# Performance work log

Measured on AMD Instinct MI355X. Metric: run time of the kernel, lower is better.

## Reference

```python
import jax, jax.numpy as jnp
import numpy as np

B, S, H, D = 8, 4096, 16, 64  # head_dim D = hidden_dim // n_heads
HID = H * D
EPS = 1e-5

def _layernorm(x, w, b):
    mu = jnp.mean(x, axis=-1, keepdims=True)
    var = jnp.var(x, axis=-1, keepdims=True)
    return (x - mu) * jax.lax.rsqrt(var + EPS) * w + b

def setup_inputs() -> dict:
    key = jax.random.key(0)
    ks = jax.random.split(key, 14)
    s = 1.0 / np.sqrt(D)
    return {
        "queries": jax.random.normal(ks[0], (B, S, HID), jnp.float32),
        "keys": jax.random.normal(ks[1], (B, S, HID), jnp.float32),
        "values": jax.random.normal(ks[2], (B, S, HID), jnp.float32),
        "memorys": jax.random.normal(ks[3], (B, H, S, D), jnp.float32),
        "Wq": jax.random.uniform(ks[4], (D, D), jnp.float32, -s, s),
        "Wk": jax.random.uniform(ks[5], (D, D), jnp.float32, -s, s),
        "Wv": jax.random.uniform(ks[6], (D, D), jnp.float32, -s, s),
        "forget_gate": jax.random.normal(ks[7], (D,), jnp.float32),
        "ln1_w": jnp.ones((D,), jnp.float32),
        "ln1_b": jnp.zeros((D,), jnp.float32),
        "W1": jax.random.uniform(ks[8], (2 * D, D), jnp.float32, -s, s),
        "ln2_w": jnp.ones((2 * D,), jnp.float32),
        "ln2_b": jnp.zeros((2 * D,), jnp.float32),
        "W2": jax.random.uniform(ks[9], (D, 2 * D), jnp.float32, -1.0 / np.sqrt(2 * D), 1.0 / np.sqrt(2 * D)),
        "b2": jax.random.uniform(ks[10], (D,), jnp.float32, -1.0 / np.sqrt(2 * D), 1.0 / np.sqrt(2 * D)),
    }

def reference(queries, keys, values, memorys, Wq, Wk, Wv, forget_gate,
              ln1_w, ln1_b, W1, ln2_w, ln2_b, W2, b2):
    # [B,S,HID] -> [B,H,S,D]
    def split_heads(x):
        return jnp.transpose(x.reshape(B, S, H, D), (0, 2, 1, 3))
    q_ = jnp.einsum('bhsd,ed->bhse', split_heads(queries), Wq)
    k_ = jnp.einsum('bhsd,ed->bhse', split_heads(keys), Wk)
    v_ = jnp.einsum('bhsd,ed->bhse', split_heads(values), Wv)
    # elementwise forget-gate memory cell
    cell = k_ * v_ + forget_gate * memorys
    cur_mem = (1.0 - forget_gate) * cell + forget_gate * memorys
    cv = q_ * cur_mem  # [B,H,S,D]
    # token mixer: LN -> Linear(D->2D, no bias) -> LN -> Linear(2D->D, bias)
    h1 = jnp.einsum('bhsd,ed->bhse', _layernorm(cv, ln1_w, ln1_b), W1)
    mixed = jnp.einsum('bhse,de->bhsd', _layernorm(h1, ln2_w, ln2_b), W2) + b2
    out = jnp.transpose(mixed, (0, 2, 1, 3)).reshape(B, S, HID)
    return out, cur_mem
```

## Files before the change

kernel.cpp:

```cpp
#include <hip/hip_runtime.h>

typedef __attribute__((ext_vector_type(4))) float f32x4;
typedef __attribute__((ext_vector_type(8))) __bf16 bf16x8;

#define MFMA(a, b, c) __builtin_amdgcn_mfma_f32_16x16x32_bf16(a, b, c, 0, 0, 0)

__device__ __forceinline__ void wave_fence() {
  asm volatile("" ::: "memory");
  __builtin_amdgcn_wave_barrier();
  asm volatile("" ::: "memory");
}

__device__ __forceinline__ bf16x8 pack8(f32x4 a, f32x4 b) {
  bf16x8 r;
  r[0] = (__bf16)a[0]; r[1] = (__bf16)a[1]; r[2] = (__bf16)a[2]; r[3] = (__bf16)a[3];
  r[4] = (__bf16)b[0]; r[5] = (__bf16)b[1]; r[6] = (__bf16)b[2]; r[7] = (__bf16)b[3];
  return r;
}

constexpr int SD  = 262144;
constexpr int HSD = 4194304;

__global__ __launch_bounds__(256, 2) void mixer_kernel(
    const float* __restrict__ Qg, const float* __restrict__ Kg,
    const float* __restrict__ Vg, const float* __restrict__ Mg,
    const float* __restrict__ Wq, const float* __restrict__ Wk,
    const float* __restrict__ Wv, const float* __restrict__ FG,
    const float* __restrict__ L1W, const float* __restrict__ L1B,
    const float* __restrict__ W1, const float* __restrict__ L2W,
    const float* __restrict__ L2B, const float* __restrict__ W2,
    const float* __restrict__ B2g, float* __restrict__ Out,
    float* __restrict__ Cm) {
  __shared__ __attribute__((aligned(16))) __bf16 lds[24576];
  const int tid = threadIdx.x;
  const int wave = tid >> 6, lane = tid & 63;
  const int c = lane & 15, g = lane >> 4;

  for (int i = tid; i < 4096; i += 256) {
    const int j = i & 7, L = (i >> 3) & 63, t = i >> 9;
    const int k = ((t >> 2) << 5) + ((L >> 4) << 3) + j;
    const int n = ((t & 3) << 4) + (L & 15);
    lds[i]         = (__bf16)Wq[n * 64 + k];
    lds[4096 + i]  = (__bf16)Wk[n * 64 + k];
    lds[8192 + i]  = (__bf16)Wv[n * 64 + k];
  }
  for (int i = tid; i < 8192; i += 256) {
    const int j = i & 7, L = (i >> 3) & 63, t = i >> 9;
    const int k = ((t >> 3) << 5) + ((L >> 4) << 3) + j;
    const int n = ((t & 7) << 4) + (L & 15);
    lds[12288 + i] = (__bf16)W1[n * 64 + k];
  }
  __syncthreads();

  float fgv[4], l1wv[4], l1bv[4], b2v[4], l2wv[8], l2bv[8];
#pragma unroll
  for (int t = 0; t < 4; ++t) {
    fgv[t]  = FG[t * 16 + c];
    l1wv[t] = L1W[t * 16 + c];
    l1bv[t] = L1B[t * 16 + c];
    b2v[t]  = B2g[t * 16 + c];
  }
#pragma unroll
  for (int t = 0; t < 8; ++t) { l2wv[t] = L2W[t * 16 + c]; l2bv[t] = L2B[t * 16 + c]; }

  bf16x8 fb2[16];
#pragma unroll
  for (int kt = 0; kt < 4; ++kt)
#pragma unroll
    for (int nt = 0; nt < 4; ++nt) {
      const float* p = W2 + (nt * 16 + c) * 128 + kt * 32 + g * 8;
      f32x4 a = *(const f32x4*)p;
      f32x4 b = *(const f32x4*)(p + 4);
      fb2[kt * 4 + nt] = pack8(a, b);
    }

  const f32x4 zf = {0.f, 0.f, 0.f, 0.f};
  const int p0 = blockIdx.x * 32;

  for (int it = 0; it < 8; ++it) {
    const int pair = p0 + it * 4 + wave;
    const int bb = pair >> 12, s = pair & 4095;

    int lz = 0;
    asm volatile("" : "+s"(lz));
    const __bf16* wl = lds + lz;
    __bf16* stg = lds + 20480 + wave * 1024 + lz;

    const float* qp = Qg + pair * 1024;
    const float* kp = Kg + pair * 1024;
    const float* vp = Vg + pair * 1024;
    const int aoff = c * 64 + g * 8;

    const f32x4 q0 = *(const f32x4*)(qp + aoff);
    const f32x4 q1 = *(const f32x4*)(qp + aoff + 4);
    const f32x4 q2 = *(const f32x4*)(qp + aoff + 32);
    const f32x4 q3 = *(const f32x4*)(qp + aoff + 36);
    const f32x4 k0 = *(const f32x4*)(kp + aoff);
    const f32x4 k1 = *(const f32x4*)(kp + aoff + 4);
    const f32x4 k2 = *(const f32x4*)(kp + aoff + 32);
    const f32x4 k3 = *(const f32x4*)(kp + aoff + 36);
    const f32x4 v0 = *(const f32x4*)(vp + aoff);
    const f32x4 v1 = *(const f32x4*)(vp + aoff + 4);
    const f32x4 v2 = *(const f32x4*)(vp + aoff + 32);
    const f32x4 v3 = *(const f32x4*)(vp + aoff + 36);

    const int mb = bb * HSD + s * 64 + c;
    float mv[4][4];
#pragma unroll
    for (int nt = 0; nt < 4; ++nt)
#pragma unroll
      for (int r = 0; r < 4; ++r)
        mv[nt][r] = Mg[mb + (g * 4 + r) * SD + nt * 16];

    const bf16x8 aq0 = pack8(q0, q1), aq1 = pack8(q2, q3);
    const bf16x8 ak0 = pack8(k0, k1), ak1 = pack8(k2, k3);
    const bf16x8 av0 = pack8(v0, v1), av1 = pack8(v2, v3);

    f32x4 accq[4], acck[4], accv[4];
#pragma unroll
    for (int nt = 0; nt < 4; ++nt) { accq[nt] = zf; acck[nt] = zf; accv[nt] = zf; }

#pragma unroll
    for (int nt = 0; nt < 4; ++nt) {
      accq[nt] = MFMA(aq0, *(const bf16x8*)(wl + nt * 512 + lane * 8), accq[nt]);
      accq[nt] = MFMA(aq1, *(const bf16x8*)(wl + (4 + nt) * 512 + lane * 8), accq[nt]);
      acck[nt] = MFMA(ak0, *(const bf16x8*)(wl + 4096 + nt * 512 + lane * 8), acck[nt]);
      acck[nt] = MFMA(ak1, *(const bf16x8*)(wl + 4096 + (4 + nt) * 512 + lane * 8), acck[nt]);
      accv[nt] = MFMA(av0, *(const bf16x8*)(wl + 8192 + nt * 512 + lane * 8), accv[nt]);
      accv[nt] = MFMA(av1, *(const bf16x8*)(wl + 8192 + (4 + nt) * 512 + lane * 8), accv[nt]);
    }

    float cv[4][4];
#pragma unroll
    for (int nt = 0; nt < 4; ++nt) {
      const float f = fgv[nt];
#pragma unroll
      for (int r = 0; r < 4; ++r) {
        const float mm = mv[nt][r];
        const float cell = acck[nt][r] * accv[nt][r] + f * mm;
        const float cm = (1.f - f) * cell + f * mm;
        Cm[mb + (g * 4 + r) * SD + nt * 16] = cm;
        cv[nt][r] = accq[nt][r] * cm;
      }
    }

    float yv[4][4];
#pragma unroll
    for (int r = 0; r < 4; ++r) {
      float s1 = cv[0][r] + cv[1][r] + cv[2][r] + cv[3][r];
      float s2 = cv[0][r] * cv[0][r] + cv[1][r] * cv[1][r] + cv[2][r] * cv[2][r] + cv[3][r] * cv[3][r];
#pragma unroll
      for (int msk = 1; msk <= 8; msk <<= 1) {
        s1 += __shfl_xor(s1, msk);
        s2 += __shfl_xor(s2, msk);
      }
      const float mu = s1 * 0.015625f;
      const float var = s2 * 0.015625f - mu * mu;
      const float rstd = rsqrtf(var + 1e-5f);
#pragma unroll
      for (int nt = 0; nt < 4; ++nt)
        yv[nt][r] = (cv[nt][r] - mu) * rstd * l1wv[nt] + l1bv[nt];
    }

    wave_fence();
#pragma unroll
    for (int nt = 0; nt < 4; ++nt)
#pragma unroll
      for (int r = 0; r < 4; ++r) {
        const int m = g * 4 + r, k = nt * 16 + c;
        stg[(m << 6) + ((((k >> 3) ^ (m & 7)) << 3)) + (k & 7)] = (__bf16)yv[nt][r];
      }
    wave_fence();
    bf16x8 a2[2];
#pragma unroll
    for (int kt = 0; kt < 2; ++kt)
      a2[kt] = *(const bf16x8*)(stg + (c << 6) + ((((kt * 4 + g) ^ (c & 7)) << 3)));

    f32x4 acch[8];
#pragma unroll
    for (int j = 0; j < 8; ++j) acch[j] = zf;
#pragma unroll
    for (int kt = 0; kt < 2; ++kt)
#pragma unroll
      for (int nt = 0; nt < 8; ++nt)
        acch[nt] = MFMA(a2[kt], *(const bf16x8*)(wl + 12288 + (kt * 8 + nt) * 512 + lane * 8), acch[nt]);

    float zz[8][4];
#pragma unroll
    for (int r = 0; r < 4; ++r) {
      float s1 = 0.f, s2 = 0.f;
#pragma unroll
      for (int j = 0; j < 8; ++j) { const float x = acch[j][r]; s1 += x; s2 += x * x; }
#pragma unroll
      for (int msk = 1; msk <= 8; msk <<= 1) {
        s1 += __shfl_xor(s1, msk);
        s2 += __shfl_xor(s2, msk);
      }
      const float mu = s1 * 0.0078125f;
      const float var = s2 * 0.0078125f - mu * mu;
      const float rstd = rsqrtf(var + 1e-5f);
#pragma unroll
      for (int j = 0; j < 8; ++j)
        zz[j][r] = (acch[j][r] - mu) * rstd * l2wv[j] + l2bv[j];
    }

    f32x4 acco[4];
#pragma unroll
    for (int nt = 0; nt < 4; ++nt) acco[nt] = zf;
#pragma unroll
    for (int half = 0; half < 2; ++half) {
      wave_fence();
#pragma unroll
      for (int jj = 0; jj < 4; ++jj)
#pragma unroll
        for (int r = 0; r < 4; ++r) {
          const int m = g * 4 + r, k = jj * 16 + c;
          stg[(m << 6) + ((((k >> 3) ^ (m & 7)) << 3)) + (k & 7)] = (__bf16)zz[half * 4 + jj][r];
        }
      wave_fence();
#pragma unroll
      for (int kk = 0; kk < 2; ++kk) {
        const bf16x8 a3 = *(const bf16x8*)(stg + (c << 6) + ((((kk * 4 + g) ^ (c & 7)) << 3)));
#pragma unroll
        for (int nt = 0; nt < 4; ++nt)
          acco[nt] = MFMA(a3, fb2[(half * 2 + kk) * 4 + nt], acco[nt]);
      }
    }

    const int ob = pair * 1024;
#pragma unroll
    for (int nt = 0; nt < 4; ++nt)
#pragma unroll
      for (int r = 0; r < 4; ++r)
        Out[ob + (g * 4 + r) * 64 + nt * 16 + c] = acco[nt][r] + b2v[nt];
  }
}

extern "C" void kernel_launch(void* const* d_in, const int* in_sizes, int n_in,
                              void* d_out, int out_size, void* d_ws, size_t ws_size,
                              hipStream_t stream) {
  const float* Qg  = (const float*)d_in[0];
  const float* Kg  = (const float*)d_in[1];
  const float* Vg  = (const float*)d_in[2];
  const float* Mg  = (const float*)d_in[3];
  const float* Wq  = (const float*)d_in[4];
  const float* Wk  = (const float*)d_in[5];
  const float* Wv  = (const float*)d_in[6];
  const float* FG  = (const float*)d_in[7];
  const float* L1W = (const float*)d_in[8];
  const float* L1B = (const float*)d_in[9];
  const float* W1  = (const float*)d_in[10];
  const float* L2W = (const float*)d_in[11];
  const float* L2B = (const float*)d_in[12];
  const float* W2  = (const float*)d_in[13];
  const float* B2g = (const float*)d_in[14];
  float* Out = (float*)d_out;
  float* Cm  = Out + 33554432;

  mixer_kernel<<<dim3(1024), dim3(256), 0, stream>>>(
      Qg, Kg, Vg, Mg, Wq, Wk, Wv, FG, L1W, L1B, W1, L2W, L2B, W2, B2g, Out, Cm);
}
```

Baseline: 654.8 us.

## Prefetch next pair's Q/K/V/memory inputs and move W2 fragments to LDS

```diff
diff --git a/kernel.cpp b/kernel.cpp
--- a/kernel.cpp
+++ b/kernel.cpp
@@ -31,10 +31,34 @@
     const float* __restrict__ L2B, const float* __restrict__ W2,
     const float* __restrict__ B2g, float* __restrict__ Out,
     float* __restrict__ Cm) {
-  __shared__ __attribute__((aligned(16))) __bf16 lds[24576];
+  __shared__ __attribute__((aligned(16))) __bf16 lds[32768];
   const int tid = threadIdx.x;
   const int wave = tid >> 6, lane = tid & 63;
   const int c = lane & 15, g = lane >> 4;
+  const int aoff = c * 64 + g * 8;
+  const int p0 = blockIdx.x * 32;
+
+  int pair = p0 + wave;
+  f32x4 q0, q1, q2, q3, k0, k1, k2, k3, v0, v1, v2, v3;
+  float mv[4][4];
+  int mb;
+  {
+    const float* qp = Qg + pair * 1024;
+    const float* kp = Kg + pair * 1024;
+    const float* vp = Vg + pair * 1024;
+    q0 = *(const f32x4*)(qp + aoff);      q1 = *(const f32x4*)(qp + aoff + 4);
+    q2 = *(const f32x4*)(qp + aoff + 32); q3 = *(const f32x4*)(qp + aoff + 36);
+    k0 = *(const f32x4*)(kp + aoff);      k1 = *(const f32x4*)(kp + aoff + 4);
+    k2 = *(const f32x4*)(kp + aoff + 32); k3 = *(const f32x4*)(kp + aoff + 36);
+    v0 = *(const f32x4*)(vp + aoff);      v1 = *(const f32x4*)(vp + aoff + 4);
+    v2 = *(const f32x4*)(vp + aoff + 32); v3 = *(const f32x4*)(vp + aoff + 36);
+    mb = (pair >> 12) * HSD + (pair & 4095) * 64 + c;
+#pragma unroll
+    for (int nt = 0; nt < 4; ++nt)
+#pragma unroll
+      for (int r = 0; r < 4; ++r)
+        mv[nt][r] = Mg[mb + (g * 4 + r) * SD + nt * 16];
+  }
 
   for (int i = tid; i < 4096; i += 256) {
     const int j = i & 7, L = (i >> 3) & 63, t = i >> 9;
@@ -46,9 +70,12 @@
   }
   for (int i = tid; i < 8192; i += 256) {
     const int j = i & 7, L = (i >> 3) & 63, t = i >> 9;
-    const int k = ((t >> 3) << 5) + ((L >> 4) << 3) + j;
-    const int n = ((t & 7) << 4) + (L & 15);
-    lds[12288 + i] = (__bf16)W1[n * 64 + k];
+    const int k1 = ((t >> 3) << 5) + ((L >> 4) << 3) + j;
+    const int n1 = ((t & 7) << 4) + (L & 15);
+    lds[12288 + i] = (__bf16)W1[n1 * 64 + k1];
+    const int k2 = ((t >> 2) << 5) + ((L >> 4) << 3) + j;
+    const int n2 = ((t & 3) << 4) + (L & 15);
+    lds[20480 + i] = (__bf16)W2[n2 * 128 + k2];
   }
   __syncthreads();
 
@@ -63,58 +90,30 @@
 #pragma unroll
   for (int t = 0; t < 8; ++t) { l2wv[t] = L2W[t * 16 + c]; l2bv[t] = L2B[t * 16 + c]; }
 
-  bf16x8 fb2[16];
-#pragma unroll
-  for (int kt = 0; kt < 4; ++kt)
-#pragma unroll
-    for (int nt = 0; nt < 4; ++nt) {
-      const float* p = W2 + (nt * 16 + c) * 128 + kt * 32 + g * 8;
-      f32x4 a = *(const f32x4*)p;
-      f32x4 b = *(const f32x4*)(p + 4);
-      fb2[kt * 4 + nt] = pack8(a, b);
-    }
-
   const f32x4 zf = {0.f, 0.f, 0.f, 0.f};
-  const int p0 = blockIdx.x * 32;
 
   for (int it = 0; it < 8; ++it) {
-    const int pair = p0 + it * 4 + wave;
-    const int bb = pair >> 12, s = pair & 4095;
-
     int lz = 0;
     asm volatile("" : "+s"(lz));
     const __bf16* wl = lds + lz;
-    __bf16* stg = lds + 20480 + wave * 1024 + lz;
-
-    const float* qp = Qg + pair * 1024;
-    const float* kp = Kg + pair * 1024;
-    const float* vp = Vg + pair * 1024;
-    const int aoff = c * 64 + g * 8;
-
-    const f32x4 q0 = *(const f32x4*)(qp + aoff);
-    const f32x4 q1 = *(const f32x4*)(qp + aoff + 4);
-    const f32x4 q2 = *(const f32x4*)(qp + aoff + 32);
-    const f32x4 q3 = *(const f32x4*)(qp + aoff + 36);
-    const f32x4 k0 = *(const f32x4*)(kp + aoff);
-    const f32x4 k1 = *(const f32x4*)(kp + aoff + 4);
-    const f32x4 k2 = *(const f32x4*)(kp + aoff + 32);
-    const f32x4 k3 = *(const f32x4*)(kp + aoff + 36);
-    const f32x4 v0 = *(const f32x4*)(vp + aoff);
-    const f32x4 v1 = *(const f32x4*)(vp + aoff + 4);
-    const f32x4 v2 = *(const f32x4*)(vp + aoff + 32);
-    const f32x4 v3 = *(const f32x4*)(vp + aoff + 36);
-
-    const int mb = bb * HSD + s * 64 + c;
-    float mv[4][4];
-#pragma unroll
-    for (int nt = 0; nt < 4; ++nt)
-#pragma unroll
-      for (int r = 0; r < 4; ++r)
-        mv[nt][r] = Mg[mb + (g * 4 + r) * SD + nt * 16];
+    __bf16* stg = lds + 28672 + wave * 1024 + lz;
 
     const bf16x8 aq0 = pack8(q0, q1), aq1 = pack8(q2, q3);
     const bf16x8 ak0 = pack8(k0, k1), ak1 = pack8(k2, k3);
     const bf16x8 av0 = pack8(v0, v1), av1 = pack8(v2, v3);
+
+    if (it < 7) {
+      const int np = pair + 4;
+      const float* qn = Qg + np * 1024;
+      const float* kn = Kg + np * 1024;
+      const float* vn = Vg + np * 1024;
+      q0 = *(const f32x4*)(qn + aoff);      q1 = *(const f32x4*)(qn + aoff + 4);
+      q2 = *(const f32x4*)(qn + aoff + 32); q3 = *(const f32x4*)(qn + aoff + 36);
+      k0 = *(const f32x4*)(kn + aoff);      k1 = *(const f32x4*)(kn + aoff + 4);
+      k2 = *(const f32x4*)(kn + aoff + 32); k3 = *(const f32x4*)(kn + aoff + 36);
+      v0 = *(const f32x4*)(vn + aoff);      v1 = *(const f32x4*)(vn + aoff + 4);
+      v2 = *(const f32x4*)(vn + aoff + 32); v3 = *(const f32x4*)(vn + aoff + 36);
+    }
 
     f32x4 accq[4], acck[4], accv[4];
 #pragma unroll
@@ -144,6 +143,16 @@
       }
     }
 
+    if (it < 7) {
+      const int np = pair + 4;
+      mb = (np >> 12) * HSD + (np & 4095) * 64 + c;
+#pragma unroll
+      for (int nt = 0; nt < 4; ++nt)
+#pragma unroll
+        for (int r = 0; r < 4; ++r)
+          mv[nt][r] = Mg[mb + (g * 4 + r) * SD + nt * 16];
+    }
+
     float yv[4][4];
 #pragma unroll
     for (int r = 0; r < 4; ++r) {
@@ -223,7 +232,7 @@
         const bf16x8 a3 = *(const bf16x8*)(stg + (c << 6) + ((((kk * 4 + g) ^ (c & 7)) << 3)));
 #pragma unroll
         for (int nt = 0; nt < 4; ++nt)
-          acco[nt] = MFMA(a3, fb2[(half * 2 + kk) * 4 + nt], acco[nt]);
+          acco[nt] = MFMA(a3, *(const bf16x8*)(wl + 20480 + ((half * 2 + kk) * 4 + nt) * 512 + lane * 8), acco[nt]);
       }
     }
 
@@ -233,6 +242,8 @@
 #pragma unroll
       for (int r = 0; r < 4; ++r)
         Out[ob + (g * 4 + r) * 64 + nt * 16 + c] = acco[nt][r] + b2v[nt];
+
+    pair += 4;
   }
 }
 
```

Result: faster. 633.9 us (-3.2%).
